# Kernel optimization log

Measured on AMD Instinct MI355X. Metric: run time of the kernel, lower is better.

Reference implementation:

```python
import jax, jax.numpy as jnp
import numpy as np

N1_SRC = 1171456  # hop-1 source nodes
N1_TGT = 45056    # hop-1 target nodes (= hop-2 source nodes)
N2_TGT = 4096     # final batch of target nodes
E1 = 1126400
E2 = 40960
IN_C, HID_C, OUT_C = 128, 256, 64


def setup_inputs() -> dict:
    key = jax.random.key(0)
    ks = jax.random.split(key, 12)
    inp = {
        "x": jax.random.normal(ks[0], (N1_SRC, IN_C), jnp.float32),
        "Wl1": jax.random.normal(ks[1], (IN_C, HID_C), jnp.float32) * (IN_C ** -0.5),
        "Wr1": jax.random.normal(ks[2], (IN_C, HID_C), jnp.float32) * (IN_C ** -0.5),
        "b1": jax.random.normal(ks[3], (HID_C,), jnp.float32) * 0.01,
        "Wl2": jax.random.normal(ks[4], (HID_C, OUT_C), jnp.float32) * (HID_C ** -0.5),
        "Wr2": jax.random.normal(ks[5], (HID_C, OUT_C), jnp.float32) * (HID_C ** -0.5),
        "b2": jax.random.normal(ks[6], (OUT_C,), jnp.float32) * 0.01,
        "src1": jax.random.randint(ks[7], (E1,), 0, N1_SRC, jnp.int32),
        "dst1": jax.random.randint(ks[8], (E1,), 0, N1_TGT, jnp.int32),
        "src2": jax.random.randint(ks[9], (E2,), 0, N1_TGT, jnp.int32),
        "dst2": jax.random.randint(ks[10], (E2,), 0, N2_TGT, jnp.int32),
    }
    return inp


def _sage_conv(x_src, x_tgt, src, dst, Wl, Wr, b, n_tgt):
    # mean aggregation of neighbor (source) features per target node
    msgs = x_src[src]                                   # [E, C] gather
    s = jax.ops.segment_sum(msgs, dst, num_segments=n_tgt)
    cnt = jax.ops.segment_sum(jnp.ones((src.shape[0],), x_src.dtype), dst,
                              num_segments=n_tgt)
    agg = s / jnp.maximum(cnt, 1.0)[:, None]
    # PyG SAGEConv: lin_l(aggregated) + lin_r(root), bias on lin_l
    return agg @ Wl + x_tgt @ Wr + b


def reference(x, Wl1, Wr1, b1, Wl2, Wr2, b2, src1, dst1, src2, dst2):
    # layer 0
    h = _sage_conv(x, x[:N1_TGT], src1, dst1, Wl1, Wr1, b1, N1_TGT)
    h = jax.nn.relu(h)  # dropout is identity in eval mode
    # layer 1
    out = _sage_conv(h, h[:N2_TGT], src2, dst2, Wl2, Wr2, b2, N2_TGT)
    return jax.nn.log_softmax(out, axis=-1)
```

## Files before the change

### kernel.cpp

```cpp
#include <hip/hip_runtime.h>
#include <hip/hip_bf16.h>

constexpr int N1_SRC = 1171456;
constexpr int N1_TGT = 45056;
constexpr int N2_TGT = 4096;
constexpr int E1 = 1126400;
constexpr int E2 = 40960;
constexpr int IN_C = 128;
constexpr int HID_C = 256;
constexpr int OUT_C = 64;
constexpr int KV = 256;

typedef __attribute__((ext_vector_type(8))) short bf16x8;
typedef __attribute__((ext_vector_type(4))) float f32x4;

__device__ __forceinline__ unsigned f2bf(float f) {
  unsigned u = __float_as_uint(f);
  return (u + 0x7FFFu + ((u >> 16) & 1u)) >> 16;
}
__device__ __forceinline__ float bf2f(unsigned u) {
  return __uint_as_float(u << 16);
}

__global__ __launch_bounds__(256) void hist(const int* __restrict__ dst,
                                            int* __restrict__ cnt, int E) {
  const int i = blockIdx.x * blockDim.x + threadIdx.x;
  if (i < E) atomicAdd(&cnt[dst[i]], 1);
}

__global__ __launch_bounds__(1024) void scan_block(const int* __restrict__ cnt,
                                                   int* __restrict__ off,
                                                   int* __restrict__ partials,
                                                   int n) {
  const int tid = threadIdx.x, lane = tid & 63, wv = tid >> 6;
  __shared__ int wsum[16];
  const int i = blockIdx.x * 1024 + tid;
  const int v = (i < n) ? cnt[i] : 0;
  int s = v;
#pragma unroll
  for (int o = 1; o < 64; o <<= 1) {
    const int t = __shfl_up(s, o);
    if (lane >= o) s += t;
  }
  if (lane == 63) wsum[wv] = s;
  __syncthreads();
  if (wv == 0 && lane < 16) {
    const int ws = wsum[lane];
    int ss = ws;
#pragma unroll
    for (int o = 1; o < 16; o <<= 1) {
      const int t = __shfl_up(ss, o);
      if (lane >= o) ss += t;
    }
    wsum[lane] = ss - ws;
  }
  __syncthreads();
  if (i < n) off[i] = wsum[wv] + s - v;
  if (tid == 1023) partials[blockIdx.x] = wsum[15] + s;
}

__global__ __launch_bounds__(64) void scan_partials(int* __restrict__ p, int nb) {
  const int t = threadIdx.x;
  const int v = (t < nb) ? p[t] : 0;
  int s = v;
#pragma unroll
  for (int o = 1; o < 64; o <<= 1) {
    const int tt = __shfl_up(s, o);
    if (t >= o) s += tt;
  }
  if (t < nb) p[t] = s - v;
}

__global__ __launch_bounds__(256) void scan_add(int* __restrict__ off,
                                                const int* __restrict__ p, int n) {
  const int i = blockIdx.x * 256 + threadIdx.x;
  if (i < n) off[i] += p[i >> 10];
}

__global__ __launch_bounds__(256) void fill_csr(
    const int* __restrict__ src, const int* __restrict__ dst,
    const int* __restrict__ off, int* __restrict__ cur,
    int* __restrict__ eidx, int E) {
  const int i = blockIdx.x * blockDim.x + threadIdx.x;
  if (i < E) {
    const int d = dst[i];
    const int p = atomicAdd(&cur[d], 1);
    eidx[off[d] + p] = src[i];
  }
}

__global__ __launch_bounds__(256) void prep_w1(const float* __restrict__ Wl1,
                                               const float* __restrict__ Wr1,
                                               unsigned short* __restrict__ Bt) {
  const int idx = blockIdx.x * 256 + threadIdx.x;
  const int k = idx & 255, n = idx >> 8;
  const float w = (k < IN_C) ? Wl1[k * HID_C + n] : Wr1[(k - IN_C) * HID_C + n];
  Bt[n * KV + k] = (unsigned short)f2bf(w);
}

__global__ __launch_bounds__(256) void prep_w2(const float* __restrict__ Wl2,
                                               const float* __restrict__ Wr2,
                                               float* __restrict__ Wl2t,
                                               float* __restrict__ Wr2t) {
  const int idx = blockIdx.x * 256 + threadIdx.x;
  const int k = idx & 255, n = idx >> 8;
  Wl2t[n * HID_C + k] = Wl2[k * OUT_C + n];
  Wr2t[n * HID_C + k] = Wr2[k * OUT_C + n];
}

__global__ __launch_bounds__(256) void conv_x(const float* __restrict__ x,
                                              unsigned short* __restrict__ Ab) {
  const size_t idx = (size_t)(blockIdx.x * 256 + threadIdx.x) * 4;
  const int m = (int)(idx >> 7);
  const int c = (int)(idx & 127);
  const float4 v = *reinterpret_cast<const float4*>(x + (size_t)m * IN_C + c);
  uint2 o;
  o.x = f2bf(v.x) | (f2bf(v.y) << 16);
  o.y = f2bf(v.z) | (f2bf(v.w) << 16);
  *reinterpret_cast<uint2*>(Ab + (size_t)m * KV + IN_C + c) = o;
}

__global__ __launch_bounds__(256) void gather1(
    const float* __restrict__ x, const int* __restrict__ eidx,
    const int* __restrict__ off, const int* __restrict__ cnt,
    unsigned short* __restrict__ Ab) {
  const int lane = threadIdx.x & 63;
  const int node = blockIdx.x * 4 + (threadIdx.x >> 6);
  const int beg = off[node];
  const int deg = cnt[node];
  float s0 = 0, s1 = 0, t0 = 0, t1 = 0, u0 = 0, u1 = 0, v0 = 0, v1 = 0;
  int i = 0;
  for (; i + 4 <= deg; i += 4) {
    const int n0 = eidx[beg + i + 0];
    const int n1 = eidx[beg + i + 1];
    const int n2 = eidx[beg + i + 2];
    const int n3 = eidx[beg + i + 3];
    const float2 a = *reinterpret_cast<const float2*>(x + (size_t)n0 * IN_C + lane * 2);
    const float2 b = *reinterpret_cast<const float2*>(x + (size_t)n1 * IN_C + lane * 2);
    const float2 c = *reinterpret_cast<const float2*>(x + (size_t)n2 * IN_C + lane * 2);
    const float2 d = *reinterpret_cast<const float2*>(x + (size_t)n3 * IN_C + lane * 2);
    s0 += a.x; s1 += a.y; t0 += b.x; t1 += b.y;
    u0 += c.x; u1 += c.y; v0 += d.x; v1 += d.y;
  }
  for (; i < deg; ++i) {
    const int n0 = eidx[beg + i];
    const float2 a = *reinterpret_cast<const float2*>(x + (size_t)n0 * IN_C + lane * 2);
    s0 += a.x; s1 += a.y;
  }
  const float inv = 1.0f / (float)(deg > 0 ? deg : 1);
  const float c0 = (s0 + t0 + u0 + v0) * inv;
  const float c1 = (s1 + t1 + u1 + v1) * inv;
  *reinterpret_cast<unsigned*>(Ab + (size_t)node * KV + lane * 2) =
      f2bf(c0) | (f2bf(c1) << 16);
}

__global__ __launch_bounds__(256) void l1_gemm(
    const unsigned short* __restrict__ Ab, const unsigned short* __restrict__ Bt,
    const float* __restrict__ b1, unsigned short* __restrict__ h_bf) {
  __shared__ unsigned short As[64 * 40];
  __shared__ unsigned short Bs[256 * 40];
  const int tid = threadIdx.x;
  const int lane = tid & 63;
  const int w = tid >> 6;
  const int r0 = blockIdx.x * 64;
  const int wn = w * 64;
  f32x4 acc[4][4] = {};
  const int arow = tid >> 2;
  const int akoff = (tid & 3) * 8;
  for (int ks = 0; ks < 8; ++ks) {
    const int k0 = ks * 32;
    if (ks) __syncthreads();
    const bf16x8 av =
        *reinterpret_cast<const bf16x8*>(Ab + (size_t)(r0 + arow) * KV + k0 + akoff);
    *reinterpret_cast<bf16x8*>(As + arow * 40 + akoff) = av;
#pragma unroll
    for (int it = 0; it < 4; ++it) {
      const int chunk = it * 256 + tid;
      const int n = chunk >> 2;
      const int koff = (chunk & 3) * 8;
      const bf16x8 bv =
          *reinterpret_cast<const bf16x8*>(Bt + (size_t)n * KV + k0 + koff);
      *reinterpret_cast<bf16x8*>(Bs + n * 40 + koff) = bv;
    }
    __syncthreads();
    const int kg = (lane >> 4) * 8;
    const int rl = lane & 15;
    bf16x8 af[4], bfr[4];
#pragma unroll
    for (int mi = 0; mi < 4; ++mi)
      af[mi] = *reinterpret_cast<const bf16x8*>(As + (mi * 16 + rl) * 40 + kg);
#pragma unroll
    for (int nj = 0; nj < 4; ++nj)
      bfr[nj] =
          *reinterpret_cast<const bf16x8*>(Bs + (wn + nj * 16 + rl) * 40 + kg);
#pragma unroll
    for (int mi = 0; mi < 4; ++mi)
#pragma unroll
      for (int nj = 0; nj < 4; ++nj)
        acc[mi][nj] = __builtin_amdgcn_mfma_f32_16x16x32_bf16(
            af[mi], bfr[nj], acc[mi][nj], 0, 0, 0);
  }
  const int rl = lane & 15;
  const int rg = lane >> 4;
#pragma unroll
  for (int nj = 0; nj < 4; ++nj) {
    const int gcol = wn + nj * 16 + rl;
    const float bias = b1[gcol];
#pragma unroll
    for (int mi = 0; mi < 4; ++mi)
#pragma unroll
      for (int r = 0; r < 4; ++r) {
        const int grow = r0 + mi * 16 + rg * 4 + r;
        const float v = fmaxf(acc[mi][nj][r] + bias, 0.0f);
        h_bf[(size_t)grow * HID_C + gcol] = (unsigned short)f2bf(v);
      }
  }
}

__global__ __launch_bounds__(256) void gather2(
    const unsigned short* __restrict__ h_bf, const int* __restrict__ eidx,
    const int* __restrict__ off, const int* __restrict__ cnt,
    float* __restrict__ agg2) {
  const int lane = threadIdx.x & 63;
  const int node = blockIdx.x * 4 + (threadIdx.x >> 6);
  const int beg = off[node];
  const int deg = cnt[node];
  float a0 = 0, a1 = 0, a2 = 0, a3 = 0, b0 = 0, b1v = 0, b2v = 0, b3 = 0;
  int i = 0;
  for (; i + 2 <= deg; i += 2) {
    const int n0 = eidx[beg + i], n1 = eidx[beg + i + 1];
    const uint2 ra =
        *reinterpret_cast<const uint2*>(h_bf + (size_t)n0 * HID_C + lane * 4);
    const uint2 rb =
        *reinterpret_cast<const uint2*>(h_bf + (size_t)n1 * HID_C + lane * 4);
    a0 += bf2f(ra.x & 0xffff); a1 += bf2f(ra.x >> 16);
    a2 += bf2f(ra.y & 0xffff); a3 += bf2f(ra.y >> 16);
    b0 += bf2f(rb.x & 0xffff); b1v += bf2f(rb.x >> 16);
    b2v += bf2f(rb.y & 0xffff); b3 += bf2f(rb.y >> 16);
  }
  if (i < deg) {
    const int n0 = eidx[beg + i];
    const uint2 ra =
        *reinterpret_cast<const uint2*>(h_bf + (size_t)n0 * HID_C + lane * 4);
    a0 += bf2f(ra.x & 0xffff); a1 += bf2f(ra.x >> 16);
    a2 += bf2f(ra.y & 0xffff); a3 += bf2f(ra.y >> 16);
  }
  const float inv = 1.0f / (float)(deg > 0 ? deg : 1);
  float4 o;
  o.x = (a0 + b0) * inv; o.y = (a1 + b1v) * inv;
  o.z = (a2 + b2v) * inv; o.w = (a3 + b3) * inv;
  *reinterpret_cast<float4*>(agg2 + (size_t)node * HID_C + lane * 4) = o;
}

__global__ __launch_bounds__(256) void l2_dense_lsm(
    const float* __restrict__ agg2, const unsigned short* __restrict__ h_bf,
    const float* __restrict__ Wl2t, const float* __restrict__ Wr2t,
    const float* __restrict__ b2, float* __restrict__ out) {
  __shared__ float Aa[16][HID_C];
  __shared__ float Ax[16][HID_C];
  const int tid = threadIdx.x;
  const int rb = blockIdx.x * 16;
#pragma unroll
  for (int it = 0; it < 4; ++it) {
    const int e = (it * 256 + tid) * 4;
    const int row = e >> 8, c = e & 255;
    *reinterpret_cast<float4*>(&Aa[row][c]) =
        *reinterpret_cast<const float4*>(agg2 + (size_t)(rb + row) * HID_C + c);
  }
#pragma unroll
  for (int it = 0; it < 2; ++it) {
    const int e = (it * 256 + tid) * 8;
    const int row = e >> 8, c = e & 255;
    const uint4 raw =
        *reinterpret_cast<const uint4*>(h_bf + (size_t)(rb + row) * HID_C + c);
    Ax[row][c + 0] = bf2f(raw.x & 0xffff); Ax[row][c + 1] = bf2f(raw.x >> 16);
    Ax[row][c + 2] = bf2f(raw.y & 0xffff); Ax[row][c + 3] = bf2f(raw.y >> 16);
    Ax[row][c + 4] = bf2f(raw.z & 0xffff); Ax[row][c + 5] = bf2f(raw.z >> 16);
    Ax[row][c + 6] = bf2f(raw.w & 0xffff); Ax[row][c + 7] = bf2f(raw.w >> 16);
  }
  __syncthreads();
  const int n = tid & 63, rg = tid >> 6;
  const float bias = b2[n];
  float acc[4] = {bias, bias, bias, bias};
  for (int k = 0; k < HID_C; k += 4) {
    const float4 wl = *reinterpret_cast<const float4*>(Wl2t + n * HID_C + k);
    const float4 wr = *reinterpret_cast<const float4*>(Wr2t + n * HID_C + k);
#pragma unroll
    for (int i = 0; i < 4; ++i) {
      const float4 av = *reinterpret_cast<const float4*>(&Aa[rg * 4 + i][k]);
      const float4 xv = *reinterpret_cast<const float4*>(&Ax[rg * 4 + i][k]);
      acc[i] += av.x * wl.x + av.y * wl.y + av.z * wl.z + av.w * wl.w +
                xv.x * wr.x + xv.y * wr.y + xv.z * wr.z + xv.w * wr.w;
    }
  }
#pragma unroll
  for (int i = 0; i < 4; ++i) {
    const float v = acc[i];
    float m = v;
#pragma unroll
    for (int o = 32; o; o >>= 1) m = fmaxf(m, __shfl_xor(m, o));
    const float e = expf(v - m);
    float s = e;
#pragma unroll
    for (int o = 32; o; o >>= 1) s += __shfl_xor(s, o);
    out[(size_t)(rb + rg * 4 + i) * OUT_C + n] = v - m - logf(s);
  }
}

extern "C" void kernel_launch(void* const* d_in, const int* in_sizes, int n_in,
                              void* d_out, int out_size, void* d_ws,
                              size_t ws_size, hipStream_t stream) {
  const float* x   = (const float*)d_in[0];
  const float* Wl1 = (const float*)d_in[1];
  const float* Wr1 = (const float*)d_in[2];
  const float* b1  = (const float*)d_in[3];
  const float* Wl2 = (const float*)d_in[4];
  const float* Wr2 = (const float*)d_in[5];
  const float* b2  = (const float*)d_in[6];
  const int* src1  = (const int*)d_in[7];
  const int* dst1  = (const int*)d_in[8];
  const int* src2  = (const int*)d_in[9];
  const int* dst2  = (const int*)d_in[10];

  char* p = (char*)d_ws;
  int* cnt1 = (int*)p;                 p += (size_t)N1_TGT * 4;
  int* cur1 = (int*)p;                 p += (size_t)N1_TGT * 4;
  int* cnt2 = (int*)p;                 p += (size_t)N2_TGT * 4;
  int* cur2 = (int*)p;                 p += (size_t)N2_TGT * 4;
  const size_t zero_bytes = (size_t)(2 * N1_TGT + 2 * N2_TGT) * 4;
  int* off1 = (int*)p;                 p += (size_t)N1_TGT * 4;
  int* off2 = (int*)p;                 p += (size_t)N2_TGT * 4;
  int* part1 = (int*)p;                p += 64 * 4;
  int* part2 = (int*)p;                p += 64 * 4;
  int* eidx1 = (int*)p;                p += (size_t)E1 * 4;
  int* eidx2 = (int*)p;                p += (size_t)E2 * 4;
  unsigned short* Bt = (unsigned short*)p;   p += (size_t)HID_C * KV * 2;
  unsigned short* Ab = (unsigned short*)p;   p += (size_t)N1_TGT * KV * 2;
  unsigned short* h_bf = (unsigned short*)p; p += (size_t)N1_TGT * HID_C * 2;
  float* agg2 = (float*)p;             p += (size_t)N2_TGT * HID_C * 4;
  float* Wl2t = (float*)p;             p += (size_t)OUT_C * HID_C * 4;
  float* Wr2t = (float*)p;             p += (size_t)OUT_C * HID_C * 4;
  float* out = (float*)d_out;

  hipMemsetAsync(d_ws, 0, zero_bytes, stream);

  prep_w1<<<dim3(256), dim3(256), 0, stream>>>(Wl1, Wr1, Bt);
  prep_w2<<<dim3(64), dim3(256), 0, stream>>>(Wl2, Wr2, Wl2t, Wr2t);
  conv_x<<<dim3(5632), dim3(256), 0, stream>>>(x, Ab);

  hist<<<dim3((E1 + 255) / 256), dim3(256), 0, stream>>>(dst1, cnt1, E1);
  scan_block<<<dim3(44), dim3(1024), 0, stream>>>(cnt1, off1, part1, N1_TGT);
  scan_partials<<<dim3(1), dim3(64), 0, stream>>>(part1, 44);
  scan_add<<<dim3(176), dim3(256), 0, stream>>>(off1, part1, N1_TGT);
  fill_csr<<<dim3((E1 + 255) / 256), dim3(256), 0, stream>>>(src1, dst1, off1,
                                                             cur1, eidx1, E1);
  gather1<<<dim3(N1_TGT / 4), dim3(256), 0, stream>>>(x, eidx1, off1, cnt1, Ab);
  l1_gemm<<<dim3(N1_TGT / 64), dim3(256), 0, stream>>>(Ab, Bt, b1, h_bf);

  hist<<<dim3((E2 + 255) / 256), dim3(256), 0, stream>>>(dst2, cnt2, E2);
  scan_block<<<dim3(4), dim3(1024), 0, stream>>>(cnt2, off2, part2, N2_TGT);
  scan_partials<<<dim3(1), dim3(64), 0, stream>>>(part2, 4);
  scan_add<<<dim3(16), dim3(256), 0, stream>>>(off2, part2, N2_TGT);
  fill_csr<<<dim3((E2 + 255) / 256), dim3(256), 0, stream>>>(src2, dst2, off2,
                                                             cur2, eidx2, E2);
  gather2<<<dim3(N2_TGT / 4), dim3(256), 0, stream>>>(h_bf, eidx2, off2, cnt2,
                                                      agg2);
  l2_dense_lsm<<<dim3(N2_TGT / 16), dim3(256), 0, stream>>>(agg2, h_bf, Wl2t,
                                                            Wr2t, b2, out);
}
```

Measured before the change: 937.1 us.

## Merge layer CSR builds, widen gather1 loads, MFMA bf16 layer-2 GEMM

Merges the per-layer histogram, scan, add and CSR fill kernels into single launches that cover both edge sets, and merges the two weight-prep kernels. gather1 now has each half-wavefront load float4 rows from alternating neighbors and combines the halves with a lane shuffle. Layer 2 stores its aggregated features as bf16 and replaces the fp32 scalar dense kernel with an MFMA bf16 GEMM whose epilogue computes log-softmax with 16-lane shuffles. The aim is to cut launch overhead, gather instruction count and layer-2 compute time, at the cost of extra bf16 rounding in layer 2.

After: 924.0 us. About the same (-1.4%).

```diff
diff --git a/kernel.cpp b/kernel.cpp
--- a/kernel.cpp
+++ b/kernel.cpp
@@ -10,6 +10,7 @@
 constexpr int HID_C = 256;
 constexpr int OUT_C = 64;
 constexpr int KV = 256;
+constexpr int KV2 = 512;
 
 typedef __attribute__((ext_vector_type(8))) short bf16x8;
 typedef __attribute__((ext_vector_type(4))) float f32x4;
@@ -22,20 +23,33 @@
   return __uint_as_float(u << 16);
 }
 
-__global__ __launch_bounds__(256) void hist(const int* __restrict__ dst,
-                                            int* __restrict__ cnt, int E) {
-  const int i = blockIdx.x * blockDim.x + threadIdx.x;
-  if (i < E) atomicAdd(&cnt[dst[i]], 1);
-}
-
-__global__ __launch_bounds__(1024) void scan_block(const int* __restrict__ cnt,
-                                                   int* __restrict__ off,
-                                                   int* __restrict__ partials,
-                                                   int n) {
+__global__ __launch_bounds__(256) void hist2(const int* __restrict__ dst1,
+                                             const int* __restrict__ dst2,
+                                             int* __restrict__ cnt1,
+                                             int* __restrict__ cnt2) {
+  const int i = blockIdx.x * 256 + threadIdx.x;
+  if (i < E1) {
+    atomicAdd(&cnt1[dst1[i]], 1);
+  } else {
+    const int j = i - E1;
+    if (j < E2) atomicAdd(&cnt2[dst2[j]], 1);
+  }
+}
+
+__global__ __launch_bounds__(1024) void scan_block2(
+    const int* __restrict__ cnt1, int* __restrict__ off1,
+    int* __restrict__ part1, const int* __restrict__ cnt2,
+    int* __restrict__ off2, int* __restrict__ part2) {
+  const int b = blockIdx.x;
+  const int* cnt;
+  int *off, *part;
+  int lb;
+  if (b < 44) { cnt = cnt1; off = off1; part = part1; lb = b; }
+  else        { cnt = cnt2; off = off2; part = part2; lb = b - 44; }
   const int tid = threadIdx.x, lane = tid & 63, wv = tid >> 6;
   __shared__ int wsum[16];
-  const int i = blockIdx.x * 1024 + tid;
-  const int v = (i < n) ? cnt[i] : 0;
+  const int i = lb * 1024 + tid;
+  const int v = cnt[i];
   int s = v;
 #pragma unroll
   for (int o = 1; o < 64; o <<= 1) {
@@ -55,12 +69,15 @@
     wsum[lane] = ss - ws;
   }
   __syncthreads();
-  if (i < n) off[i] = wsum[wv] + s - v;
-  if (tid == 1023) partials[blockIdx.x] = wsum[15] + s;
-}
-
-__global__ __launch_bounds__(64) void scan_partials(int* __restrict__ p, int nb) {
-  const int t = threadIdx.x;
+  off[i] = wsum[wv] + s - v;
+  if (tid == 1023) part[lb] = wsum[15] + s;
+}
+
+__global__ __launch_bounds__(128) void scan_partials2(int* __restrict__ part1,
+                                                      int* __restrict__ part2) {
+  const int wv = threadIdx.x >> 6, t = threadIdx.x & 63;
+  int* p = wv ? part2 : part1;
+  const int nb = wv ? 4 : 44;
   const int v = (t < nb) ? p[t] : 0;
   int s = v;
 #pragma unroll
@@ -71,41 +88,56 @@
   if (t < nb) p[t] = s - v;
 }
 
-__global__ __launch_bounds__(256) void scan_add(int* __restrict__ off,
-                                                const int* __restrict__ p, int n) {
+__global__ __launch_bounds__(256) void scan_add2(int* __restrict__ off1,
+                                                 const int* __restrict__ part1,
+                                                 int* __restrict__ off2,
+                                                 const int* __restrict__ part2) {
+  const int b = blockIdx.x;
+  if (b < 176) {
+    const int i = b * 256 + threadIdx.x;
+    off1[i] += part1[i >> 10];
+  } else {
+    const int i = (b - 176) * 256 + threadIdx.x;
+    off2[i] += part2[i >> 10];
+  }
+}
+
+__global__ __launch_bounds__(256) void fill2(
+    const int* __restrict__ src1, const int* __restrict__ dst1,
+    const int* __restrict__ off1, int* __restrict__ cur1,
+    int* __restrict__ eidx1, const int* __restrict__ src2,
+    const int* __restrict__ dst2, const int* __restrict__ off2,
+    int* __restrict__ cur2, int* __restrict__ eidx2) {
   const int i = blockIdx.x * 256 + threadIdx.x;
-  if (i < n) off[i] += p[i >> 10];
-}
-
-__global__ __launch_bounds__(256) void fill_csr(
-    const int* __restrict__ src, const int* __restrict__ dst,
-    const int* __restrict__ off, int* __restrict__ cur,
-    int* __restrict__ eidx, int E) {
-  const int i = blockIdx.x * blockDim.x + threadIdx.x;
-  if (i < E) {
-    const int d = dst[i];
-    const int p = atomicAdd(&cur[d], 1);
-    eidx[off[d] + p] = src[i];
-  }
-}
-
-__global__ __launch_bounds__(256) void prep_w1(const float* __restrict__ Wl1,
-                                               const float* __restrict__ Wr1,
-                                               unsigned short* __restrict__ Bt) {
+  if (i < E1) {
+    const int d = dst1[i];
+    const int p = atomicAdd(&cur1[d], 1);
+    eidx1[off1[d] + p] = src1[i];
+  } else {
+    const int j = i - E1;
+    if (j < E2) {
+      const int d = dst2[j];
+      const int p = atomicAdd(&cur2[d], 1);
+      eidx2[off2[d] + p] = src2[j];
+    }
+  }
+}
+
+__global__ __launch_bounds__(256) void prep_w(
+    const float* __restrict__ Wl1, const float* __restrict__ Wr1,
+    const float* __restrict__ Wl2, const float* __restrict__ Wr2,
+    unsigned short* __restrict__ Bt, unsigned short* __restrict__ B2t) {
   const int idx = blockIdx.x * 256 + threadIdx.x;
-  const int k = idx & 255, n = idx >> 8;
-  const float w = (k < IN_C) ? Wl1[k * HID_C + n] : Wr1[(k - IN_C) * HID_C + n];
-  Bt[n * KV + k] = (unsigned short)f2bf(w);
-}
-
-__global__ __launch_bounds__(256) void prep_w2(const float* __restrict__ Wl2,
-                                               const float* __restrict__ Wr2,
-                                               float* __restrict__ Wl2t,
-                                               float* __restrict__ Wr2t) {
-  const int idx = blockIdx.x * 256 + threadIdx.x;
-  const int k = idx & 255, n = idx >> 8;
-  Wl2t[n * HID_C + k] = Wl2[k * OUT_C + n];
-  Wr2t[n * HID_C + k] = Wr2[k * OUT_C + n];
+  if (idx < 65536) {
+    const int k = idx & 255, n = idx >> 8;
+    const float w = (k < IN_C) ? Wl1[k * HID_C + n] : Wr1[(k - IN_C) * HID_C + n];
+    Bt[n * KV + k] = (unsigned short)f2bf(w);
+  } else {
+    const int j = idx - 65536;
+    const int k = j & 511, n = j >> 9;
+    const float w = (k < HID_C) ? Wl2[k * OUT_C + n] : Wr2[(k - HID_C) * OUT_C + n];
+    B2t[n * KV2 + k] = (unsigned short)f2bf(w);
+  }
 }
 
 __global__ __launch_bounds__(256) void conv_x(const float* __restrict__ x,
@@ -125,33 +157,55 @@
     const int* __restrict__ off, const int* __restrict__ cnt,
     unsigned short* __restrict__ Ab) {
   const int lane = threadIdx.x & 63;
+  const int half = lane >> 5;
+  const int c4 = (lane & 31) * 4;
   const int node = blockIdx.x * 4 + (threadIdx.x >> 6);
   const int beg = off[node];
   const int deg = cnt[node];
-  float s0 = 0, s1 = 0, t0 = 0, t1 = 0, u0 = 0, u1 = 0, v0 = 0, v1 = 0;
+  float s0 = 0, s1 = 0, s2 = 0, s3 = 0;
+  float t0 = 0, t1 = 0, t2 = 0, t3 = 0;
+  float u0 = 0, u1 = 0, u2 = 0, u3 = 0;
+  float v0 = 0, v1 = 0, v2 = 0, v3 = 0;
   int i = 0;
-  for (; i + 4 <= deg; i += 4) {
-    const int n0 = eidx[beg + i + 0];
-    const int n1 = eidx[beg + i + 1];
-    const int n2 = eidx[beg + i + 2];
-    const int n3 = eidx[beg + i + 3];
-    const float2 a = *reinterpret_cast<const float2*>(x + (size_t)n0 * IN_C + lane * 2);
-    const float2 b = *reinterpret_cast<const float2*>(x + (size_t)n1 * IN_C + lane * 2);
-    const float2 c = *reinterpret_cast<const float2*>(x + (size_t)n2 * IN_C + lane * 2);
-    const float2 d = *reinterpret_cast<const float2*>(x + (size_t)n3 * IN_C + lane * 2);
-    s0 += a.x; s1 += a.y; t0 += b.x; t1 += b.y;
-    u0 += c.x; u1 += c.y; v0 += d.x; v1 += d.y;
-  }
-  for (; i < deg; ++i) {
+  for (; i + 8 <= deg; i += 8) {
+    const int n0 = eidx[beg + i + 0 + half];
+    const int n1 = eidx[beg + i + 2 + half];
+    const int n2 = eidx[beg + i + 4 + half];
+    const int n3 = eidx[beg + i + 6 + half];
+    const float4 a = *reinterpret_cast<const float4*>(x + (size_t)n0 * IN_C + c4);
+    const float4 b = *reinterpret_cast<const float4*>(x + (size_t)n1 * IN_C + c4);
+    const float4 c = *reinterpret_cast<const float4*>(x + (size_t)n2 * IN_C + c4);
+    const float4 d = *reinterpret_cast<const float4*>(x + (size_t)n3 * IN_C + c4);
+    s0 += a.x; s1 += a.y; s2 += a.z; s3 += a.w;
+    t0 += b.x; t1 += b.y; t2 += b.z; t3 += b.w;
+    u0 += c.x; u1 += c.y; u2 += c.z; u3 += c.w;
+    v0 += d.x; v1 += d.y; v2 += d.z; v3 += d.w;
+  }
+  for (; i + 2 <= deg; i += 2) {
+    const int n0 = eidx[beg + i + half];
+    const float4 a = *reinterpret_cast<const float4*>(x + (size_t)n0 * IN_C + c4);
+    s0 += a.x; s1 += a.y; s2 += a.z; s3 += a.w;
+  }
+  if (i < deg && half == 0) {
     const int n0 = eidx[beg + i];
-    const float2 a = *reinterpret_cast<const float2*>(x + (size_t)n0 * IN_C + lane * 2);
-    s0 += a.x; s1 += a.y;
-  }
-  const float inv = 1.0f / (float)(deg > 0 ? deg : 1);
-  const float c0 = (s0 + t0 + u0 + v0) * inv;
-  const float c1 = (s1 + t1 + u1 + v1) * inv;
-  *reinterpret_cast<unsigned*>(Ab + (size_t)node * KV + lane * 2) =
-      f2bf(c0) | (f2bf(c1) << 16);
+    const float4 a = *reinterpret_cast<const float4*>(x + (size_t)n0 * IN_C + c4);
+    s0 += a.x; s1 += a.y; s2 += a.z; s3 += a.w;
+  }
+  float r0 = (s0 + t0) + (u0 + v0);
+  float r1 = (s1 + t1) + (u1 + v1);
+  float r2 = (s2 + t2) + (u2 + v2);
+  float r3 = (s3 + t3) + (u3 + v3);
+  r0 += __shfl_xor(r0, 32);
+  r1 += __shfl_xor(r1, 32);
+  r2 += __shfl_xor(r2, 32);
+  r3 += __shfl_xor(r3, 32);
+  if (half == 0) {
+    const float inv = 1.0f / (float)(deg > 0 ? deg : 1);
+    uint2 o;
+    o.x = f2bf(r0 * inv) | (f2bf(r1 * inv) << 16);
+    o.y = f2bf(r2 * inv) | (f2bf(r3 * inv) << 16);
+    *reinterpret_cast<uint2*>(Ab + (size_t)node * KV + c4) = o;
+  }
 }
 
 __global__ __launch_bounds__(256) void l1_gemm(
@@ -220,7 +274,7 @@
 __global__ __launch_bounds__(256) void gather2(
     const unsigned short* __restrict__ h_bf, const int* __restrict__ eidx,
     const int* __restrict__ off, const int* __restrict__ cnt,
-    float* __restrict__ agg2) {
+    unsigned short* __restrict__ agg2_bf) {
   const int lane = threadIdx.x & 63;
   const int node = blockIdx.x * 4 + (threadIdx.x >> 6);
   const int beg = off[node];
@@ -246,64 +300,56 @@
     a2 += bf2f(ra.y & 0xffff); a3 += bf2f(ra.y >> 16);
   }
   const float inv = 1.0f / (float)(deg > 0 ? deg : 1);
-  float4 o;
-  o.x = (a0 + b0) * inv; o.y = (a1 + b1v) * inv;
-  o.z = (a2 + b2v) * inv; o.w = (a3 + b3) * inv;
-  *reinterpret_cast<float4*>(agg2 + (size_t)node * HID_C + lane * 4) = o;
-}
-
-__global__ __launch_bounds__(256) void l2_dense_lsm(
-    const float* __restrict__ agg2, const unsigned short* __restrict__ h_bf,
-    const float* __restrict__ Wl2t, const float* __restrict__ Wr2t,
-    const float* __restrict__ b2, float* __restrict__ out) {
-  __shared__ float Aa[16][HID_C];
-  __shared__ float Ax[16][HID_C];
-  const int tid = threadIdx.x;
-  const int rb = blockIdx.x * 16;
-#pragma unroll
-  for (int it = 0; it < 4; ++it) {
-    const int e = (it * 256 + tid) * 4;
-    const int row = e >> 8, c = e & 255;
-    *reinterpret_cast<float4*>(&Aa[row][c]) =
-        *reinterpret_cast<const float4*>(agg2 + (size_t)(rb + row) * HID_C + c);
-  }
-#pragma unroll
-  for (int it = 0; it < 2; ++it) {
-    const int e = (it * 256 + tid) * 8;
-    const int row = e >> 8, c = e & 255;
-    const uint4 raw =
-        *reinterpret_cast<const uint4*>(h_bf + (size_t)(rb + row) * HID_C + c);
-    Ax[row][c + 0] = bf2f(raw.x & 0xffff); Ax[row][c + 1] = bf2f(raw.x >> 16);
-    Ax[row][c + 2] = bf2f(raw.y & 0xffff); Ax[row][c + 3] = bf2f(raw.y >> 16);
-    Ax[row][c + 4] = bf2f(raw.z & 0xffff); Ax[row][c + 5] = bf2f(raw.z >> 16);
-    Ax[row][c + 6] = bf2f(raw.w & 0xffff); Ax[row][c + 7] = bf2f(raw.w >> 16);
-  }
-  __syncthreads();
-  const int n = tid & 63, rg = tid >> 6;
-  const float bias = b2[n];
-  float acc[4] = {bias, bias, bias, bias};
-  for (int k = 0; k < HID_C; k += 4) {
-    const float4 wl = *reinterpret_cast<const float4*>(Wl2t + n * HID_C + k);
-    const float4 wr = *reinterpret_cast<const float4*>(Wr2t + n * HID_C + k);
-#pragma unroll
-    for (int i = 0; i < 4; ++i) {
-      const float4 av = *reinterpret_cast<const float4*>(&Aa[rg * 4 + i][k]);
-      const float4 xv = *reinterpret_cast<const float4*>(&Ax[rg * 4 + i][k]);
-      acc[i] += av.x * wl.x + av.y * wl.y + av.z * wl.z + av.w * wl.w +
-                xv.x * wr.x + xv.y * wr.y + xv.z * wr.z + xv.w * wr.w;
+  uint2 o;
+  o.x = f2bf((a0 + b0) * inv) | (f2bf((a1 + b1v) * inv) << 16);
+  o.y = f2bf((a2 + b2v) * inv) | (f2bf((a3 + b3) * inv) << 16);
+  *reinterpret_cast<uint2*>(agg2_bf + (size_t)node * HID_C + lane * 4) = o;
+}
+
+__global__ __launch_bounds__(256) void l2_gemm_lsm(
+    const unsigned short* __restrict__ agg2_bf,
+    const unsigned short* __restrict__ h_bf,
+    const unsigned short* __restrict__ B2t, const float* __restrict__ b2,
+    float* __restrict__ out) {
+  const int lane = threadIdx.x & 63;
+  const int wv = threadIdx.x >> 6;
+  const int r0 = blockIdx.x * 64 + wv * 16;
+  const int rl = lane & 15;
+  const int kg = (lane >> 4) * 8;
+  f32x4 acc[4] = {};
+#pragma unroll
+  for (int phase = 0; phase < 2; ++phase) {
+    const unsigned short* __restrict__ A = phase ? h_bf : agg2_bf;
+#pragma unroll
+    for (int ks = 0; ks < 8; ++ks) {
+      const int k0 = ks * 32;
+      const bf16x8 af =
+          *reinterpret_cast<const bf16x8*>(A + (size_t)(r0 + rl) * HID_C + k0 + kg);
+#pragma unroll
+      for (int nj = 0; nj < 4; ++nj) {
+        const bf16x8 bf_ = *reinterpret_cast<const bf16x8*>(
+            B2t + (size_t)(nj * 16 + rl) * KV2 + phase * HID_C + k0 + kg);
+        acc[nj] = __builtin_amdgcn_mfma_f32_16x16x32_bf16(af, bf_, acc[nj], 0, 0, 0);
+      }
     }
   }
-#pragma unroll
-  for (int i = 0; i < 4; ++i) {
-    const float v = acc[i];
-    float m = v;
-#pragma unroll
-    for (int o = 32; o; o >>= 1) m = fmaxf(m, __shfl_xor(m, o));
-    const float e = expf(v - m);
-    float s = e;
-#pragma unroll
-    for (int o = 32; o; o >>= 1) s += __shfl_xor(s, o);
-    out[(size_t)(rb + rg * 4 + i) * OUT_C + n] = v - m - logf(s);
+  const int rg = lane >> 4;
+#pragma unroll
+  for (int r = 0; r < 4; ++r) {
+    float v[4];
+#pragma unroll
+    for (int nj = 0; nj < 4; ++nj) v[nj] = acc[nj][r] + b2[nj * 16 + rl];
+    float m = fmaxf(fmaxf(v[0], v[1]), fmaxf(v[2], v[3]));
+#pragma unroll
+    for (int o = 1; o < 16; o <<= 1) m = fmaxf(m, __shfl_xor(m, o));
+    float s = expf(v[0] - m) + expf(v[1] - m) + expf(v[2] - m) + expf(v[3] - m);
+#pragma unroll
+    for (int o = 1; o < 16; o <<= 1) s += __shfl_xor(s, o);
+    const float lse = m + logf(s);
+    const int grow = r0 + rg * 4 + r;
+#pragma unroll
+    for (int nj = 0; nj < 4; ++nj)
+      out[(size_t)grow * OUT_C + nj * 16 + rl] = v[nj] - lse;
   }
 }
 
@@ -334,37 +380,31 @@
   int* part2 = (int*)p;                p += 64 * 4;
   int* eidx1 = (int*)p;                p += (size_t)E1 * 4;
   int* eidx2 = (int*)p;                p += (size_t)E2 * 4;
-  unsigned short* Bt = (unsigned short*)p;   p += (size_t)HID_C * KV * 2;
-  unsigned short* Ab = (unsigned short*)p;   p += (size_t)N1_TGT * KV * 2;
-  unsigned short* h_bf = (unsigned short*)p; p += (size_t)N1_TGT * HID_C * 2;
-  float* agg2 = (float*)p;             p += (size_t)N2_TGT * HID_C * 4;
-  float* Wl2t = (float*)p;             p += (size_t)OUT_C * HID_C * 4;
-  float* Wr2t = (float*)p;             p += (size_t)OUT_C * HID_C * 4;
+  unsigned short* Bt = (unsigned short*)p;      p += (size_t)HID_C * KV * 2;
+  unsigned short* B2t = (unsigned short*)p;     p += (size_t)OUT_C * KV2 * 2;
+  unsigned short* Ab = (unsigned short*)p;      p += (size_t)N1_TGT * KV * 2;
+  unsigned short* h_bf = (unsigned short*)p;    p += (size_t)N1_TGT * HID_C * 2;
+  unsigned short* agg2_bf = (unsigned short*)p; p += (size_t)N2_TGT * HID_C * 2;
   float* out = (float*)d_out;
 
   hipMemsetAsync(d_ws, 0, zero_bytes, stream);
 
-  prep_w1<<<dim3(256), dim3(256), 0, stream>>>(Wl1, Wr1, Bt);
-  prep_w2<<<dim3(64), dim3(256), 0, stream>>>(Wl2, Wr2, Wl2t, Wr2t);
+  prep_w<<<dim3(384), dim3(256), 0, stream>>>(Wl1, Wr1, Wl2, Wr2, Bt, B2t);
   conv_x<<<dim3(5632), dim3(256), 0, stream>>>(x, Ab);
 
-  hist<<<dim3((E1 + 255) / 256), dim3(256), 0, stream>>>(dst1, cnt1, E1);
-  scan_block<<<dim3(44), dim3(1024), 0, stream>>>(cnt1, off1, part1, N1_TGT);
-  scan_partials<<<dim3(1), dim3(64), 0, stream>>>(part1, 44);
-  scan_add<<<dim3(176), dim3(256), 0, stream>>>(off1, part1, N1_TGT);
-  fill_csr<<<dim3((E1 + 255) / 256), dim3(256), 0, stream>>>(src1, dst1, off1,
-                                                             cur1, eidx1, E1);
+  hist2<<<dim3(4560), dim3(256), 0, stream>>>(dst1, dst2, cnt1, cnt2);
+  scan_block2<<<dim3(48), dim3(1024), 0, stream>>>(cnt1, off1, part1, cnt2,
+                                                   off2, part2);
+  scan_partials2<<<dim3(1), dim3(128), 0, stream>>>(part1, part2);
+  scan_add2<<<dim3(192), dim3(256), 0, stream>>>(off1, part1, off2, part2);
+  fill2<<<dim3(4560), dim3(256), 0, stream>>>(src1, dst1, off1, cur1, eidx1,
+                                              src2, dst2, off2, cur2, eidx2);
+
   gather1<<<dim3(N1_TGT / 4), dim3(256), 0, stream>>>(x, eidx1, off1, cnt1, Ab);
   l1_gemm<<<dim3(N1_TGT / 64), dim3(256), 0, stream>>>(Ab, Bt, b1, h_bf);
 
-  hist<<<dim3((E2 + 255) / 256), dim3(256), 0, stream>>>(dst2, cnt2, E2);
-  scan_block<<<dim3(4), dim3(1024), 0, stream>>>(cnt2, off2, part2, N2_TGT);
-  scan_partials<<<dim3(1), dim3(64), 0, stream>>>(part2, 4);
-  scan_add<<<dim3(16), dim3(256), 0, stream>>>(off2, part2, N2_TGT);
-  fill_csr<<<dim3((E2 + 255) / 256), dim3(256), 0, stream>>>(src2, dst2, off2,
-                                                             cur2, eidx2, E2);
   gather2<<<dim3(N2_TGT / 4), dim3(256), 0, stream>>>(h_bf, eidx2, off2, cnt2,
-                                                      agg2);
-  l2_dense_lsm<<<dim3(N2_TGT / 16), dim3(256), 0, stream>>>(agg2, h_bf, Wl2t,
-                                                            Wr2t, b2, out);
-}
+                                                      agg2_bf);
+  l2_gemm_lsm<<<dim3(N2_TGT / 64), dim3(256), 0, stream>>>(agg2_bf, h_bf, B2t,
+                                                           b2, out);
+}
```
